# Performance work log

Measured on AMD Instinct MI355X. Metric: run time of the kernel, lower is better.

Reference implementation:

```python
import jax, jax.numpy as jnp
import numpy as np

B, C, DE, DE1 = 64, 80, 300, 1024
J, S = 4000, 100            # JOINT_EMB_SIZE, pooling_stride
K = J // S                  # out_in_tmp = 40
FDIM = 2048                 # IMAGE_CHANNEL / CLASSIFIER_CHANNEL


def setup_inputs() -> dict:
    key = jax.random.key(0)
    ks = jax.random.split(key, 14)
    sc = 0.02
    return {
        "feature": jax.random.normal(ks[0], (B, FDIM, 14, 14), jnp.float32),
        "inp": jax.random.normal(ks[1], (C, DE), jnp.float32),
        # A-branch 1x1 convs (Conv2d(300,1024,k=1) == linear over channel dim)
        "Wb1": jax.random.normal(ks[2], (DE1, DE), jnp.float32) * sc,
        "bb1": jnp.zeros((DE1,), jnp.float32),
        "Wb2": jax.random.normal(ks[3], (DE1, DE), jnp.float32) * sc,
        "bb2": jnp.zeros((DE1,), jnp.float32),
        # GCN weights (uniform(-1/sqrt(out), ..) as in reset_parameters)
        "Wg1": jax.random.uniform(ks[4], (DE, 1024), jnp.float32, -1/np.sqrt(1024), 1/np.sqrt(1024)),
        "Wg2": jax.random.uniform(ks[5], (1024, FDIM), jnp.float32, -1/np.sqrt(FDIM), 1/np.sqrt(FDIM)),
        # MFB projections
        "Wimg": jax.random.normal(ks[6], (J, FDIM), jnp.float32) * sc,
        "bimg": jnp.zeros((J,), jnp.float32),
        "Wcls": jax.random.normal(ks[7], (J, FDIM), jnp.float32) * sc,
        "bcls": jnp.zeros((J,), jnp.float32),
        # ML_fc_layer: Linear(C*K, C)
        "Wml": jax.random.normal(ks[8], (C, C * K), jnp.float32) * sc,
        "bml": jnp.zeros((C,), jnp.float32),
    }


def _forward(feature, inp, Wb1, bb1, Wb2, bb2, Wg1, Wg2, Wimg, bimg, Wcls, bcls, Wml, bml):
    # backbone output -> MaxPool2d(14,14) -> [B, 2048]
    feat = jnp.max(feature, axis=(2, 3))
    # inp.view(1, d_e, num_classes, 1): raw row-major reshape (NOT transpose)
    X = inp.reshape(DE, C)                               # [300, 80]
    b1 = jax.nn.sigmoid(Wb1 @ X + bb1[:, None])          # [1024, 80]
    b2 = jax.nn.sigmoid(Wb2 @ X + bb2[:, None])
    A = (b1.T @ b2) / float(C)                           # [80, 80]
    I = jnp.eye(C, dtype=A.dtype)
    A_wave = A + I
    d = A_wave.sum(axis=1) ** -0.5
    d = jnp.where(jnp.isfinite(d), d, 0.0)
    A_hat = d[:, None] * A_wave * d[None, :]             # D^-1/2 A~ D^-1/2
    L_A_loss = jnp.abs(A_hat - I).sum()
    # GCN layers
    h = jax.nn.leaky_relu(A_hat @ (inp @ Wg1), 0.2)      # [80, 1024]
    x = A_hat @ (h @ Wg2)                                # [80, 2048]
    # MFB bilinear pooling, fully batched (dropout off / eval mode)
    img = feat @ Wimg.T + bimg                           # [B, J]
    cls = x @ Wcls.T + bcls                              # [C, J]
    pooled = jnp.einsum('bks,cks->bck', img.reshape(B, K, S), cls.reshape(C, K, S))
    out = pooled.reshape(B, C * K) @ Wml.T + bml         # [B, C]
    return out, L_A_loss


def reference(feature, inp, Wb1, bb1, Wb2, bb2, Wg1, Wg2, Wimg, bimg, Wcls, bcls, Wml, bml):
    return _forward(feature, inp, Wb1, bb1, Wb2, bb2, Wg1, Wg2, Wimg, bimg, Wcls, bcls, Wml, bml)
```

## Files before the change

kernel.cpp:

```cpp
#include <hip/hip_runtime.h>
#include <math.h>

#define B_    64
#define C_    80
#define DE_   300
#define DE1_  1024
#define J_    4000
#define S_    100
#define KP_   40
#define FDIM_ 2048

#define WS_FEAT   0
#define WS_B1     131072
#define WS_B2     212992
#define WS_AW     294912
#define WS_AHAT   301312
#define WS_T1     307712
#define WS_H      389632
#define WS_HH     471552
#define WS_X      553472
#define WS_IMG    717312
#define WS_CLS    973312
#define WS_POOL   1293312

typedef __bf16 bf16x8 __attribute__((ext_vector_type(8)));
typedef float  f32x4  __attribute__((ext_vector_type(4)));

__device__ __forceinline__ bf16x8 cvt_bf16x8(float4 a, float4 b) {
    bf16x8 r;
    r[0] = (__bf16)a.x; r[1] = (__bf16)a.y; r[2] = (__bf16)a.z; r[3] = (__bf16)a.w;
    r[4] = (__bf16)b.x; r[5] = (__bf16)b.y; r[6] = (__bf16)b.z; r[7] = (__bf16)b.w;
    return r;
}

__global__ void init_kernel(float* __restrict__ x, float* __restrict__ Aw) {
    int idx = blockIdx.x * 256 + threadIdx.x;
    if (idx < 163840) { x[idx] = 0.0f; return; }
    idx -= 163840;
    if (idx < 6400) {
        int i = idx / 80, j = idx % 80;
        Aw[idx] = (i == j) ? 1.0f : 0.0f;
    }
}

__global__ void maxpool_kernel(const float* __restrict__ feature,
                               float* __restrict__ feat) {
    int gtid = blockIdx.x * 256 + threadIdx.x;
    int wid  = gtid >> 6;
    int lane = gtid & 63;
    const float* src = feature + (size_t)wid * 196;
    float v = -INFINITY;
    if (lane < 49) {
        float4 u = ((const float4*)src)[lane];
        v = fmaxf(fmaxf(u.x, u.y), fmaxf(u.z, u.w));
    }
    #pragma unroll
    for (int off = 32; off > 0; off >>= 1)
        v = fmaxf(v, __shfl_down(v, off));
    if (lane == 0) feat[wid] = v;
}

__global__ void b1b2_kernel(const float* __restrict__ inp,
                            const float* __restrict__ Wb1, const float* __restrict__ bb1,
                            const float* __restrict__ Wb2, const float* __restrict__ bb2,
                            float* __restrict__ b1, float* __restrict__ b2) {
    int idx = blockIdx.x * 256 + threadIdx.x;
    int which = idx >= 81920;
    int r = which ? idx - 81920 : idx;
    int o = r / 80, c = r % 80;
    const float* W = which ? Wb2 : Wb1;
    const float* bb = which ? bb2 : bb1;
    float acc = bb[o];
    const float* wrow = W + o * 300;
    for (int k = 0; k < 300; ++k)
        acc = fmaf(wrow[k], inp[k * 80 + c], acc);
    float s = 1.0f / (1.0f + expf(-acc));
    (which ? b2 : b1)[r] = s;
}

__global__ void gram_kernel(const float* __restrict__ b1,
                            const float* __restrict__ b2,
                            float* __restrict__ Aw) {
    int idx = blockIdx.x * 256 + threadIdx.x;
    int i = idx / 80, j = idx % 80;
    int k0 = blockIdx.y * 256;
    float acc = 0.f;
    for (int k = k0; k < k0 + 256; ++k)
        acc = fmaf(b1[k * 80 + i], b2[k * 80 + j], acc);
    atomicAdd(&Aw[idx], acc * (1.0f / 80.0f));
}

__global__ void ahat_kernel(const float* __restrict__ Aw,
                            float* __restrict__ Ahat,
                            float* __restrict__ loss_out) {
    __shared__ float dsh[80];
    __shared__ float red[256];
    int tid = threadIdx.x;
    if (tid < 80) {
        float rs = 0.f;
        for (int j = 0; j < 80; ++j) rs += Aw[tid * 80 + j];
        float dv = rsqrtf(rs);
        if (!isfinite(dv)) dv = 0.f;
        dsh[tid] = dv;
    }
    __syncthreads();
    float loss = 0.f;
    for (int idx = tid; idx < 6400; idx += 256) {
        int i = idx / 80, j = idx % 80;
        float ah = dsh[i] * Aw[idx] * dsh[j];
        Ahat[idx] = ah;
        loss += fabsf(ah - (i == j ? 1.0f : 0.0f));
    }
    red[tid] = loss;
    __syncthreads();
    for (int s = 128; s > 0; s >>= 1) {
        if (tid < s) red[tid] += red[tid + s];
        __syncthreads();
    }
    if (tid == 0) *loss_out = red[0];
}

__global__ void t1_kernel(const float* __restrict__ inp,
                          const float* __restrict__ Wg1,
                          float* __restrict__ t1) {
    int idx = blockIdx.x * 256 + threadIdx.x;
    int m = idx >> 10, n = idx & 1023;
    float acc = 0.f;
    const float* arow = inp + m * 300;
    for (int k = 0; k < 300; ++k)
        acc = fmaf(arow[k], Wg1[k * 1024 + n], acc);
    t1[idx] = acc;
}

__global__ void h_kernel(const float* __restrict__ Ahat,
                         const float* __restrict__ t1,
                         float* __restrict__ h) {
    int idx = blockIdx.x * 256 + threadIdx.x;
    int m = idx >> 10, n = idx & 1023;
    float acc = 0.f;
    const float* arow = Ahat + m * 80;
    for (int k = 0; k < 80; ++k)
        acc = fmaf(arow[k], t1[k * 1024 + n], acc);
    h[idx] = acc > 0.f ? acc : 0.2f * acc;
}

__global__ void hh_kernel(const float* __restrict__ Ahat,
                          const float* __restrict__ h,
                          float* __restrict__ hh) {
    int idx = blockIdx.x * 256 + threadIdx.x;
    int m = idx >> 10, n = idx & 1023;
    float acc = 0.f;
    const float* arow = Ahat + m * 80;
    for (int k = 0; k < 80; ++k)
        acc = fmaf(arow[k], h[k * 1024 + n], acc);
    hh[idx] = acc;
}

__global__ __launch_bounds__(320) void gemm_x_mfma(const float* __restrict__ hh,
                                                   const float* __restrict__ Wg2,
                                                   float* __restrict__ x) {
    int w = threadIdx.x >> 6;
    int lane = threadIdx.x & 63;
    int r = lane & 15, q = lane >> 4;
    int n0 = blockIdx.x * 32;
    int k0base = blockIdx.y * 512;
    int m0 = w * 16;

    const float* arow = hh + (size_t)(m0 + r) * 1024 + k0base + q * 8;
    const float* bcol = Wg2 + (size_t)(k0base + q * 8) * 2048 + n0 + r;

    f32x4 acc0 = {0.f, 0.f, 0.f, 0.f}, acc1 = {0.f, 0.f, 0.f, 0.f};
    for (int ks = 0; ks < 16; ++ks) {
        float4 a0 = *(const float4*)(arow + ks * 32);
        float4 a1 = *(const float4*)(arow + ks * 32 + 4);
        bf16x8 afrag = cvt_bf16x8(a0, a1);
        const float* bp = bcol + (size_t)ks * 32 * 2048;
        bf16x8 bf0, bf1;
        #pragma unroll
        for (int j = 0; j < 8; ++j) {
            bf0[j] = (__bf16)bp[(size_t)j * 2048];
            bf1[j] = (__bf16)bp[(size_t)j * 2048 + 16];
        }
        acc0 = __builtin_amdgcn_mfma_f32_16x16x32_bf16(afrag, bf0, acc0, 0, 0, 0);
        acc1 = __builtin_amdgcn_mfma_f32_16x16x32_bf16(afrag, bf1, acc1, 0, 0, 0);
    }
    #pragma unroll
    for (int i = 0; i < 4; ++i) {
        int row = m0 + q * 4 + i;
        atomicAdd(&x[(size_t)row * 2048 + n0 + r], acc0[i]);
        atomicAdd(&x[(size_t)row * 2048 + n0 + 16 + r], acc1[i]);
    }
}

__global__ __launch_bounds__(320) void gemm_imgcls_mfma(
        const float* __restrict__ feat, const float* __restrict__ Wimg,
        const float* __restrict__ bimg,
        const float* __restrict__ x, const float* __restrict__ Wcls,
        const float* __restrict__ bcls,
        float* __restrict__ img, float* __restrict__ cls) {
    int role = blockIdx.y;
    int w = threadIdx.x >> 6;
    if (role == 0 && w >= 4) return;
    int lane = threadIdx.x & 63;
    int r = lane & 15, q = lane >> 4;
    int n0 = blockIdx.x * 32;
    int m0 = w * 16;

    const float* A    = role ? x    : feat;
    const float* W    = role ? Wcls : Wimg;
    const float* bias = role ? bcls : bimg;
    float* Cout       = role ? cls  : img;

    const float4* arow = (const float4*)(A + (size_t)(m0 + r) * 2048 + q * 8);
    const float4* b0row = (const float4*)(W + (size_t)(n0 + r) * 2048 + q * 8);
    const float4* b1row = (const float4*)(W + (size_t)(n0 + 16 + r) * 2048 + q * 8);

    f32x4 acc0 = {0.f, 0.f, 0.f, 0.f}, acc1 = {0.f, 0.f, 0.f, 0.f};
    for (int ks = 0; ks < 64; ++ks) {
        float4 a0 = arow[ks * 8], a1 = arow[ks * 8 + 1];
        float4 b00 = b0row[ks * 8], b01 = b0row[ks * 8 + 1];
        float4 b10 = b1row[ks * 8], b11 = b1row[ks * 8 + 1];
        bf16x8 afrag = cvt_bf16x8(a0, a1);
        bf16x8 bf0 = cvt_bf16x8(b00, b01);
        bf16x8 bf1 = cvt_bf16x8(b10, b11);
        acc0 = __builtin_amdgcn_mfma_f32_16x16x32_bf16(afrag, bf0, acc0, 0, 0, 0);
        acc1 = __builtin_amdgcn_mfma_f32_16x16x32_bf16(afrag, bf1, acc1, 0, 0, 0);
    }
    float bia0 = bias[n0 + r];
    float bia1 = bias[n0 + 16 + r];
    #pragma unroll
    for (int i = 0; i < 4; ++i) {
        int row = m0 + q * 4 + i;
        Cout[(size_t)row * 4000 + n0 + r]      = acc0[i] + bia0;
        Cout[(size_t)row * 4000 + n0 + 16 + r] = acc1[i] + bia1;
    }
}

__global__ void pool_kernel(const float* __restrict__ img,
                            const float* __restrict__ cls,
                            float* __restrict__ pooled) {
    int idx = blockIdx.x * 256 + threadIdx.x;
    int b = idx / 3200;
    int rem = idx % 3200;
    int c = rem / 40, k = rem % 40;
    const float4* ia = (const float4*)(img + (size_t)b * 4000 + k * 100);
    const float4* ca = (const float4*)(cls + (size_t)c * 4000 + k * 100);
    float acc = 0.f;
    #pragma unroll 5
    for (int s = 0; s < 25; ++s) {
        float4 u = ia[s], v = ca[s];
        acc = fmaf(u.x, v.x, acc);
        acc = fmaf(u.y, v.y, acc);
        acc = fmaf(u.z, v.z, acc);
        acc = fmaf(u.w, v.w, acc);
    }
    pooled[(size_t)b * 3200 + c * 40 + k] = acc;
}

__global__ void out_kernel(const float* __restrict__ pooled,
                           const float* __restrict__ Wml,
                           const float* __restrict__ bml,
                           float* __restrict__ out) {
    int gid = blockIdx.x * 256 + threadIdx.x;
    int wid = gid >> 6;
    int lane = gid & 63;
    int b = wid / 80, co = wid % 80;
    const float* pr = pooled + (size_t)b * 3200;
    const float* wr = Wml + (size_t)co * 3200;
    float acc = 0.f;
    for (int k = lane; k < 3200; k += 64)
        acc = fmaf(pr[k], wr[k], acc);
    #pragma unroll
    for (int off = 32; off > 0; off >>= 1)
        acc += __shfl_down(acc, off);
    if (lane == 0) out[wid] = acc + bml[co];
}

extern "C" void kernel_launch(void* const* d_in, const int* in_sizes, int n_in,
                              void* d_out, int out_size, void* d_ws, size_t ws_size,
                              hipStream_t stream) {
    const float* feature = (const float*)d_in[0];
    const float* inp     = (const float*)d_in[1];
    const float* Wb1     = (const float*)d_in[2];
    const float* bb1     = (const float*)d_in[3];
    const float* Wb2     = (const float*)d_in[4];
    const float* bb2     = (const float*)d_in[5];
    const float* Wg1     = (const float*)d_in[6];
    const float* Wg2     = (const float*)d_in[7];
    const float* Wimg    = (const float*)d_in[8];
    const float* bimg    = (const float*)d_in[9];
    const float* Wcls    = (const float*)d_in[10];
    const float* bcls    = (const float*)d_in[11];
    const float* Wml     = (const float*)d_in[12];
    const float* bml     = (const float*)d_in[13];

    float* ws  = (float*)d_ws;
    float* out = (float*)d_out;

    float* feat   = ws + WS_FEAT;
    float* b1     = ws + WS_B1;
    float* b2     = ws + WS_B2;
    float* Aw     = ws + WS_AW;
    float* Ahat   = ws + WS_AHAT;
    float* t1     = ws + WS_T1;
    float* h      = ws + WS_H;
    float* hh     = ws + WS_HH;
    float* x      = ws + WS_X;
    float* img    = ws + WS_IMG;
    float* cls    = ws + WS_CLS;
    float* pooled = ws + WS_POOL;

    init_kernel<<<666, 256, 0, stream>>>(x, Aw);
    maxpool_kernel<<<32768, 256, 0, stream>>>(feature, feat);
    b1b2_kernel<<<640, 256, 0, stream>>>(inp, Wb1, bb1, Wb2, bb2, b1, b2);
    gram_kernel<<<dim3(25, 4), 256, 0, stream>>>(b1, b2, Aw);
    ahat_kernel<<<1, 256, 0, stream>>>(Aw, Ahat, out + 5120);
    t1_kernel<<<320, 256, 0, stream>>>(inp, Wg1, t1);
    h_kernel<<<320, 256, 0, stream>>>(Ahat, t1, h);
    hh_kernel<<<320, 256, 0, stream>>>(Ahat, h, hh);
    gemm_x_mfma<<<dim3(64, 2), 320, 0, stream>>>(hh, Wg2, x);
    gemm_imgcls_mfma<<<dim3(125, 2), 320, 0, stream>>>(feat, Wimg, bimg, x, Wcls, bcls, img, cls);
    pool_kernel<<<800, 256, 0, stream>>>(img, cls, pooled);
    out_kernel<<<1280, 256, 0, stream>>>(pooled, Wml, bml, out);
}
```

Measured before the change: 369.8 us.

## Fuse init/maxpool and independent GEMMs, split-K the MFMA GEMMs with atomics

Merges the zero/bias initialisation into the maxpool launch, and merges the b1/b2 projection, the inp@Wg1 product and the feat@Wimg GEMM into one launch. This cuts the kernel count and lets independent work run concurrently. The t1, img, cls and x GEMMs are split along K into more blocks that accumulate with atomics into bias-initialised buffers, which raises parallelism on the long-K projections. Several loops also get unroll pragmas and the gram kernel gets a finer K split. The cost is more atomic traffic and non-deterministic summation order.

Result: faster. 349.3 us (-5.5%).

```diff
diff --git a/kernel.cpp b/kernel.cpp
--- a/kernel.cpp
+++ b/kernel.cpp
@@ -33,49 +33,126 @@
     return r;
 }
 
-__global__ void init_kernel(float* __restrict__ x, float* __restrict__ Aw) {
-    int idx = blockIdx.x * 256 + threadIdx.x;
+template<int KSTEPS>
+__device__ __forceinline__ void mfma_bt_tile(const float* __restrict__ A0,
+                                             const float* __restrict__ B0,
+                                             const float* __restrict__ B1,
+                                             f32x4& acc0, f32x4& acc1) {
+    #pragma unroll 4
+    for (int ks = 0; ks < KSTEPS; ++ks) {
+        const float4* ap = (const float4*)(A0 + ks * 32);
+        const float4* b0 = (const float4*)(B0 + ks * 32);
+        const float4* b1 = (const float4*)(B1 + ks * 32);
+        float4 a0 = ap[0], a1 = ap[1];
+        float4 b00 = b0[0], b01 = b0[1];
+        float4 b10 = b1[0], b11 = b1[1];
+        bf16x8 af  = cvt_bf16x8(a0, a1);
+        bf16x8 bf0 = cvt_bf16x8(b00, b01);
+        bf16x8 bf1 = cvt_bf16x8(b10, b11);
+        acc0 = __builtin_amdgcn_mfma_f32_16x16x32_bf16(af, bf0, acc0, 0, 0, 0);
+        acc1 = __builtin_amdgcn_mfma_f32_16x16x32_bf16(af, bf1, acc1, 0, 0, 0);
+    }
+}
+
+__device__ __forceinline__ void mfma_store_atomic(float* __restrict__ C, int Nst,
+                                                  int m0, int n0, int r, int q,
+                                                  const f32x4& acc0, const f32x4& acc1) {
+    #pragma unroll
+    for (int i = 0; i < 4; ++i) {
+        int row = m0 + q * 4 + i;
+        atomicAdd(&C[(size_t)row * Nst + n0 + r], acc0[i]);
+        atomicAdd(&C[(size_t)row * Nst + n0 + 16 + r], acc1[i]);
+    }
+}
+
+__global__ void fused_init_maxpool(const float* __restrict__ feature,
+                                   float* __restrict__ feat,
+                                   float* __restrict__ x, float* __restrict__ Aw,
+                                   float* __restrict__ t1,
+                                   const float* __restrict__ bimg, float* __restrict__ img,
+                                   const float* __restrict__ bcls, float* __restrict__ cls) {
+    if (blockIdx.x < 32768) {
+        int gtid = blockIdx.x * 256 + threadIdx.x;
+        int wid  = gtid >> 6;
+        int lane = gtid & 63;
+        const float* src = feature + (size_t)wid * 196;
+        float v = -INFINITY;
+        if (lane < 49) {
+            float4 u = ((const float4*)src)[lane];
+            v = fmaxf(fmaxf(u.x, u.y), fmaxf(u.z, u.w));
+        }
+        #pragma unroll
+        for (int off = 32; off > 0; off >>= 1)
+            v = fmaxf(v, __shfl_down(v, off));
+        if (lane == 0) feat[wid] = v;
+        return;
+    }
+    int idx = (blockIdx.x - 32768) * 256 + threadIdx.x;
     if (idx < 163840) { x[idx] = 0.0f; return; }
     idx -= 163840;
     if (idx < 6400) {
         int i = idx / 80, j = idx % 80;
         Aw[idx] = (i == j) ? 1.0f : 0.0f;
-    }
-}
-
-__global__ void maxpool_kernel(const float* __restrict__ feature,
-                               float* __restrict__ feat) {
-    int gtid = blockIdx.x * 256 + threadIdx.x;
-    int wid  = gtid >> 6;
-    int lane = gtid & 63;
-    const float* src = feature + (size_t)wid * 196;
-    float v = -INFINITY;
-    if (lane < 49) {
-        float4 u = ((const float4*)src)[lane];
-        v = fmaxf(fmaxf(u.x, u.y), fmaxf(u.z, u.w));
-    }
-    #pragma unroll
-    for (int off = 32; off > 0; off >>= 1)
-        v = fmaxf(v, __shfl_down(v, off));
-    if (lane == 0) feat[wid] = v;
-}
-
-__global__ void b1b2_kernel(const float* __restrict__ inp,
-                            const float* __restrict__ Wb1, const float* __restrict__ bb1,
-                            const float* __restrict__ Wb2, const float* __restrict__ bb2,
-                            float* __restrict__ b1, float* __restrict__ b2) {
-    int idx = blockIdx.x * 256 + threadIdx.x;
-    int which = idx >= 81920;
-    int r = which ? idx - 81920 : idx;
-    int o = r / 80, c = r % 80;
-    const float* W = which ? Wb2 : Wb1;
-    const float* bb = which ? bb2 : bb1;
-    float acc = bb[o];
-    const float* wrow = W + o * 300;
-    for (int k = 0; k < 300; ++k)
-        acc = fmaf(wrow[k], inp[k * 80 + c], acc);
-    float s = 1.0f / (1.0f + expf(-acc));
-    (which ? b2 : b1)[r] = s;
+        return;
+    }
+    idx -= 6400;
+    if (idx < 81920) { t1[idx] = 0.0f; return; }
+    idx -= 81920;
+    if (idx < 256000) { img[idx] = bimg[idx % 4000]; return; }
+    idx -= 256000;
+    if (idx < 320000) { cls[idx] = bcls[idx % 4000]; }
+}
+
+__global__ void fused_stage2(const float* __restrict__ inp,
+                             const float* __restrict__ Wb1, const float* __restrict__ bb1,
+                             const float* __restrict__ Wb2, const float* __restrict__ bb2,
+                             float* __restrict__ b1, float* __restrict__ b2,
+                             const float* __restrict__ Wg1, float* __restrict__ t1,
+                             const float* __restrict__ feat, const float* __restrict__ Wimg,
+                             float* __restrict__ img) {
+    int bid = blockIdx.x;
+    if (bid < 640) {
+        int idx = bid * 256 + threadIdx.x;
+        int which = idx >= 81920;
+        int r = which ? idx - 81920 : idx;
+        int o = r / 80, c = r % 80;
+        const float* W = which ? Wb2 : Wb1;
+        const float* bb = which ? bb2 : bb1;
+        float acc = bb[o];
+        const float* wrow = W + o * 300;
+        #pragma unroll 10
+        for (int k = 0; k < 300; ++k)
+            acc = fmaf(wrow[k], inp[k * 80 + c], acc);
+        float s = 1.0f / (1.0f + expf(-acc));
+        (which ? b2 : b1)[r] = s;
+        return;
+    }
+    if (bid < 1920) {
+        int bid2 = bid - 640;
+        int chunk = bid2 / 320, blk = bid2 % 320;
+        int idx = blk * 256 + threadIdx.x;
+        int m = idx >> 10, n = idx & 1023;
+        float acc = 0.f;
+        const float* arow = inp + m * 300;
+        int k0 = chunk * 75;
+        #pragma unroll 5
+        for (int k = k0; k < k0 + 75; ++k)
+            acc = fmaf(arow[k], Wg1[k * 1024 + n], acc);
+        atomicAdd(&t1[idx], acc);
+        return;
+    }
+    int bid3 = bid - 1920;
+    int nt = bid3 % 125, kc = bid3 / 125;
+    int w = threadIdx.x >> 6;
+    int lane = threadIdx.x & 63;
+    int r = lane & 15, q = lane >> 4;
+    int n0 = nt * 32, m0 = w * 16, k0 = kc * 512;
+    const float* A0 = feat + (size_t)(m0 + r) * 2048 + k0 + q * 8;
+    const float* B0 = Wimg + (size_t)(n0 + r) * 2048 + k0 + q * 8;
+    const float* B1 = Wimg + (size_t)(n0 + 16 + r) * 2048 + k0 + q * 8;
+    f32x4 acc0 = {0.f, 0.f, 0.f, 0.f}, acc1 = {0.f, 0.f, 0.f, 0.f};
+    mfma_bt_tile<16>(A0, B0, B1, acc0, acc1);
+    mfma_store_atomic(img, 4000, m0, n0, r, q, acc0, acc1);
 }
 
 __global__ void gram_kernel(const float* __restrict__ b1,
@@ -83,9 +160,10 @@
                             float* __restrict__ Aw) {
     int idx = blockIdx.x * 256 + threadIdx.x;
     int i = idx / 80, j = idx % 80;
-    int k0 = blockIdx.y * 256;
-    float acc = 0.f;
-    for (int k = k0; k < k0 + 256; ++k)
+    int k0 = blockIdx.y * 128;
+    float acc = 0.f;
+    #pragma unroll 8
+    for (int k = k0; k < k0 + 128; ++k)
         acc = fmaf(b1[k * 80 + i], b2[k * 80 + j], acc);
     atomicAdd(&Aw[idx], acc * (1.0f / 80.0f));
 }
@@ -98,6 +176,7 @@
     int tid = threadIdx.x;
     if (tid < 80) {
         float rs = 0.f;
+        #pragma unroll 8
         for (int j = 0; j < 80; ++j) rs += Aw[tid * 80 + j];
         float dv = rsqrtf(rs);
         if (!isfinite(dv)) dv = 0.f;
@@ -120,18 +199,6 @@
     if (tid == 0) *loss_out = red[0];
 }
 
-__global__ void t1_kernel(const float* __restrict__ inp,
-                          const float* __restrict__ Wg1,
-                          float* __restrict__ t1) {
-    int idx = blockIdx.x * 256 + threadIdx.x;
-    int m = idx >> 10, n = idx & 1023;
-    float acc = 0.f;
-    const float* arow = inp + m * 300;
-    for (int k = 0; k < 300; ++k)
-        acc = fmaf(arow[k], Wg1[k * 1024 + n], acc);
-    t1[idx] = acc;
-}
-
 __global__ void h_kernel(const float* __restrict__ Ahat,
                          const float* __restrict__ t1,
                          float* __restrict__ h) {
@@ -139,6 +206,7 @@
     int m = idx >> 10, n = idx & 1023;
     float acc = 0.f;
     const float* arow = Ahat + m * 80;
+    #pragma unroll 8
     for (int k = 0; k < 80; ++k)
         acc = fmaf(arow[k], t1[k * 1024 + n], acc);
     h[idx] = acc > 0.f ? acc : 0.2f * acc;
@@ -151,6 +219,7 @@
     int m = idx >> 10, n = idx & 1023;
     float acc = 0.f;
     const float* arow = Ahat + m * 80;
+    #pragma unroll 8
     for (int k = 0; k < 80; ++k)
         acc = fmaf(arow[k], h[k * 1024 + n], acc);
     hh[idx] = acc;
@@ -163,14 +232,15 @@
     int lane = threadIdx.x & 63;
     int r = lane & 15, q = lane >> 4;
     int n0 = blockIdx.x * 32;
-    int k0base = blockIdx.y * 512;
+    int k0 = blockIdx.y * 256;
     int m0 = w * 16;
 
-    const float* arow = hh + (size_t)(m0 + r) * 1024 + k0base + q * 8;
-    const float* bcol = Wg2 + (size_t)(k0base + q * 8) * 2048 + n0 + r;
+    const float* arow = hh + (size_t)(m0 + r) * 1024 + k0 + q * 8;
+    const float* bcol = Wg2 + (size_t)(k0 + q * 8) * 2048 + n0 + r;
 
     f32x4 acc0 = {0.f, 0.f, 0.f, 0.f}, acc1 = {0.f, 0.f, 0.f, 0.f};
-    for (int ks = 0; ks < 16; ++ks) {
+    #pragma unroll 2
+    for (int ks = 0; ks < 8; ++ks) {
         float4 a0 = *(const float4*)(arow + ks * 32);
         float4 a1 = *(const float4*)(arow + ks * 32 + 4);
         bf16x8 afrag = cvt_bf16x8(a0, a1);
@@ -184,56 +254,24 @@
         acc0 = __builtin_amdgcn_mfma_f32_16x16x32_bf16(afrag, bf0, acc0, 0, 0, 0);
         acc1 = __builtin_amdgcn_mfma_f32_16x16x32_bf16(afrag, bf1, acc1, 0, 0, 0);
     }
-    #pragma unroll
-    for (int i = 0; i < 4; ++i) {
-        int row = m0 + q * 4 + i;
-        atomicAdd(&x[(size_t)row * 2048 + n0 + r], acc0[i]);
-        atomicAdd(&x[(size_t)row * 2048 + n0 + 16 + r], acc1[i]);
-    }
-}
-
-__global__ __launch_bounds__(320) void gemm_imgcls_mfma(
-        const float* __restrict__ feat, const float* __restrict__ Wimg,
-        const float* __restrict__ bimg,
-        const float* __restrict__ x, const float* __restrict__ Wcls,
-        const float* __restrict__ bcls,
-        float* __restrict__ img, float* __restrict__ cls) {
-    int role = blockIdx.y;
+    mfma_store_atomic(x, 2048, m0, n0, r, q, acc0, acc1);
+}
+
+__global__ __launch_bounds__(320) void gemm_cls_mfma(const float* __restrict__ x,
+                                                     const float* __restrict__ Wcls,
+                                                     float* __restrict__ cls) {
     int w = threadIdx.x >> 6;
-    if (role == 0 && w >= 4) return;
     int lane = threadIdx.x & 63;
     int r = lane & 15, q = lane >> 4;
     int n0 = blockIdx.x * 32;
+    int k0 = blockIdx.y * 512;
     int m0 = w * 16;
-
-    const float* A    = role ? x    : feat;
-    const float* W    = role ? Wcls : Wimg;
-    const float* bias = role ? bcls : bimg;
-    float* Cout       = role ? cls  : img;
-
-    const float4* arow = (const float4*)(A + (size_t)(m0 + r) * 2048 + q * 8);
-    const float4* b0row = (const float4*)(W + (size_t)(n0 + r) * 2048 + q * 8);
-    const float4* b1row = (const float4*)(W + (size_t)(n0 + 16 + r) * 2048 + q * 8);
-
+    const float* A0 = x    + (size_t)(m0 + r) * 2048 + k0 + q * 8;
+    const float* B0 = Wcls + (size_t)(n0 + r) * 2048 + k0 + q * 8;
+    const float* B1 = Wcls + (size_t)(n0 + 16 + r) * 2048 + k0 + q * 8;
     f32x4 acc0 = {0.f, 0.f, 0.f, 0.f}, acc1 = {0.f, 0.f, 0.f, 0.f};
-    for (int ks = 0; ks < 64; ++ks) {
-        float4 a0 = arow[ks * 8], a1 = arow[ks * 8 + 1];
-        float4 b00 = b0row[ks * 8], b01 = b0row[ks * 8 + 1];
-        float4 b10 = b1row[ks * 8], b11 = b1row[ks * 8 + 1];
-        bf16x8 afrag = cvt_bf16x8(a0, a1);
-        bf16x8 bf0 = cvt_bf16x8(b00, b01);
-        bf16x8 bf1 = cvt_bf16x8(b10, b11);
-        acc0 = __builtin_amdgcn_mfma_f32_16x16x32_bf16(afrag, bf0, acc0, 0, 0, 0);
-        acc1 = __builtin_amdgcn_mfma_f32_16x16x32_bf16(afrag, bf1, acc1, 0, 0, 0);
-    }
-    float bia0 = bias[n0 + r];
-    float bia1 = bias[n0 + 16 + r];
-    #pragma unroll
-    for (int i = 0; i < 4; ++i) {
-        int row = m0 + q * 4 + i;
-        Cout[(size_t)row * 4000 + n0 + r]      = acc0[i] + bia0;
-        Cout[(size_t)row * 4000 + n0 + 16 + r] = acc1[i] + bia1;
-    }
+    mfma_bt_tile<16>(A0, B0, B1, acc0, acc1);
+    mfma_store_atomic(cls, 4000, m0, n0, r, q, acc0, acc1);
 }
 
 __global__ void pool_kernel(const float* __restrict__ img,
@@ -268,6 +306,7 @@
     const float* pr = pooled + (size_t)b * 3200;
     const float* wr = Wml + (size_t)co * 3200;
     float acc = 0.f;
+    #pragma unroll 5
     for (int k = lane; k < 3200; k += 64)
         acc = fmaf(pr[k], wr[k], acc);
     #pragma unroll
@@ -310,16 +349,16 @@
     float* cls    = ws + WS_CLS;
     float* pooled = ws + WS_POOL;
 
-    init_kernel<<<666, 256, 0, stream>>>(x, Aw);
-    maxpool_kernel<<<32768, 256, 0, stream>>>(feature, feat);
-    b1b2_kernel<<<640, 256, 0, stream>>>(inp, Wb1, bb1, Wb2, bb2, b1, b2);
-    gram_kernel<<<dim3(25, 4), 256, 0, stream>>>(b1, b2, Aw);
+    fused_init_maxpool<<<36003, 256, 0, stream>>>(feature, feat, x, Aw, t1,
+                                                  bimg, img, bcls, cls);
+    fused_stage2<<<2420, 256, 0, stream>>>(inp, Wb1, bb1, Wb2, bb2, b1, b2,
+                                           Wg1, t1, feat, Wimg, img);
+    gram_kernel<<<dim3(25, 8), 256, 0, stream>>>(b1, b2, Aw);
     ahat_kernel<<<1, 256, 0, stream>>>(Aw, Ahat, out + 5120);
-    t1_kernel<<<320, 256, 0, stream>>>(inp, Wg1, t1);
     h_kernel<<<320, 256, 0, stream>>>(Ahat, t1, h);
     hh_kernel<<<320, 256, 0, stream>>>(Ahat, h, hh);
-    gemm_x_mfma<<<dim3(64, 2), 320, 0, stream>>>(hh, Wg2, x);
-    gemm_imgcls_mfma<<<dim3(125, 2), 320, 0, stream>>>(feat, Wimg, bimg, x, Wcls, bcls, img, cls);
+    gemm_x_mfma<<<dim3(64, 4), 320, 0, stream>>>(hh, Wg2, x);
+    gemm_cls_mfma<<<dim3(125, 4), 320, 0, stream>>>(x, Wcls, cls);
     pool_kernel<<<800, 256, 0, stream>>>(img, cls, pooled);
     out_kernel<<<1280, 256, 0, stream>>>(pooled, Wml, bml, out);
 }
```
